# Kernel optimization log

Hardware: AMD Instinct MI355X
Metric: run time of the kernel (lower is better)

The kernel has to match this reference:

```python
import jax, jax.numpy as jnp
import numpy as np

K = 2  # kernel_size == stride (non-overlapping pool)

def setup_inputs() -> dict:
    key = jax.random.key(0)
    x = jax.random.normal(key, (32, 128, 128, 128), dtype=jnp.float32)
    return {"x": x}

def reference(x) -> jnp.ndarray:
    B, C, H, W = x.shape
    h, w = H // K, W // K
    # extract non-overlapping KxK patches: [B,C,h,w,K*K], row-major within window
    p = x.reshape(B, C, h, K, w, K).transpose(0, 1, 2, 4, 3, 5).reshape(B, C, h, w, K * K)
    vals = jnp.max(p, axis=-1)            # pooled values [B,C,h,w]
    idx = jnp.argmax(p, axis=-1)          # in-window flat index (first max, like torch)
    # decode global position of the max element
    row = jnp.arange(h, dtype=jnp.int32)[:, None] * K + (idx // K)  # [B,C,h,w]
    col = jnp.arange(w, dtype=jnp.int32)[None, :] * K + (idx % K)
    pos_h = row.astype(x.dtype) / H
    pos_w = col.astype(x.dtype) / W
    return jnp.concatenate([vals, pos_h, pos_w], axis=1)  # [B, 3C, h, w]
```

## Files before the change

kernel.cpp:

```cpp
#include <hip/hip_runtime.h>


typedef float f32x4 __attribute__((ext_vector_type(4)));
typedef float f32x2 __attribute__((ext_vector_type(2)));

__global__ __launch_bounds__(256) void pap_kernel(const float* __restrict__ x,
                                                  float* __restrict__ out) {
    constexpr int C = 128, H = 128, W = 128;
    constexpr int OH = 64, OW = 64;
    constexpr float inv = 1.0f / 128.0f;
    constexpr int NTILES = 32 * C * (OH / 2);
    constexpr size_t plane = (size_t)C * OH * OW;

    const int lane = threadIdx.x & 63;
    const int wid  = (blockIdx.x * blockDim.x + threadIdx.x) >> 6;
    const int nw   = (gridDim.x * blockDim.x) >> 6;
    const bool hi  = lane >= 32;
    const int j    = lane & 31;

    for (int t = wid; t < NTILES; t += nw) {
        const int oh01 = t & 31;
        const int bc   = t >> 5;

        const size_t base = (size_t)bc * (H * W) + (size_t)oh01 * (4 * W) + lane * 4;
        f32x4 la = __builtin_nontemporal_load(reinterpret_cast<const f32x4*>(x + base));
        f32x4 lb = __builtin_nontemporal_load(reinterpret_cast<const f32x4*>(x + base + 2 * W));

        float top[4], bot[4];
        #pragma unroll
        for (int k = 0; k < 4; ++k) {
            const float sa = __shfl_xor(la[k], 32, 64);
            const float sb = __shfl_xor(lb[k], 32, 64);
            top[k] = hi ? sb : la[k];
            bot[k] = hi ? lb[k] : sa;
        }

        const int oh_out = 2 * oh01 + (hi ? 1 : 0);
        f32x2 vals, ph, pw;
        {
            float v = top[0]; int idx = 0;
            if (top[1] > v) { v = top[1]; idx = 1; }
            if (bot[0] > v) { v = bot[0]; idx = 2; }
            if (bot[1] > v) { v = bot[1]; idx = 3; }
            vals.x = v;
            ph.x = (float)(2 * oh_out + (idx >> 1)) * inv;
            pw.x = (float)(4 * j + (idx & 1)) * inv;
        }
        {
            float v = top[2]; int idx = 0;
            if (top[3] > v) { v = top[3]; idx = 1; }
            if (bot[2] > v) { v = bot[2]; idx = 2; }
            if (bot[3] > v) { v = bot[3]; idx = 3; }
            vals.y = v;
            ph.y = (float)(2 * oh_out + (idx >> 1)) * inv;
            pw.y = (float)(4 * j + 2 + (idx & 1)) * inv;
        }

        const int b_ = bc >> 7, c = bc & (C - 1);
        const size_t orow = ((size_t)(b_ * (3 * C) + c)) * (OH * OW)
                          + (size_t)oh_out * OW + 2 * j;
        __builtin_nontemporal_store(vals, reinterpret_cast<f32x2*>(out + orow));
        __builtin_nontemporal_store(ph,   reinterpret_cast<f32x2*>(out + orow + plane));
        __builtin_nontemporal_store(pw,   reinterpret_cast<f32x2*>(out + orow + 2 * plane));
    }
}

extern "C" void kernel_launch(void* const* d_in, const int* in_sizes, int n_in,
                              void* d_out, int out_size, void* d_ws, size_t ws_size,
                              hipStream_t stream) {
    const float* x = (const float*)d_in[0];
    float* out = (float*)d_out;
    const int blocks = 4096;
    pap_kernel<<<blocks, 256, 0, stream>>>(x, out);
}
```

Baseline: 82.76 us.

## Use fixed per-wave batch stride with hoisted index math and unrolled loads

Result: slower. 87.05 us (+5.2%).

```diff
diff --git a/kernel.cpp b/kernel.cpp
--- a/kernel.cpp
+++ b/kernel.cpp
@@ -9,33 +9,44 @@
     constexpr int C = 128, H = 128, W = 128;
     constexpr int OH = 64, OW = 64;
     constexpr float inv = 1.0f / 128.0f;
-    constexpr int NTILES = 32 * C * (OH / 2);
     constexpr size_t plane = (size_t)C * OH * OW;
+    constexpr int NITER = 16;
+    constexpr size_t IN_STEP  = (size_t)256 * H * W;
+    constexpr size_t OUT_STEP = (size_t)2 * 3 * C * OH * OW;
 
     const int lane = threadIdx.x & 63;
     const int wid  = (blockIdx.x * blockDim.x + threadIdx.x) >> 6;
-    const int nw   = (gridDim.x * blockDim.x) >> 6;
     const bool hi  = lane >= 32;
     const int j    = lane & 31;
 
-    for (int t = wid; t < NTILES; t += nw) {
-        const int oh01 = t & 31;
-        const int bc   = t >> 5;
+    const int oh01 = wid & 31;
+    const int bc0  = wid >> 5;
+    const int b0   = bc0 >> 7, c0 = bc0 & (C - 1);
+    const int oh_out = 2 * oh01 + (hi ? 1 : 0);
 
-        const size_t base = (size_t)bc * (H * W) + (size_t)oh01 * (4 * W) + lane * 4;
+    size_t base = (size_t)bc0 * (H * W) + (size_t)oh01 * (4 * W) + lane * 4;
+    size_t orow = ((size_t)(b0 * (3 * C) + c0)) * (OH * OW)
+                + (size_t)oh_out * OW + 2 * j;
+
+    const float ph_lo = (float)(2 * oh_out) * inv;
+    const float ph_hi = (float)(2 * oh_out + 1) * inv;
+    const float pw0_lo = (float)(4 * j) * inv,     pw0_hi = (float)(4 * j + 1) * inv;
+    const float pw1_lo = (float)(4 * j + 2) * inv, pw1_hi = (float)(4 * j + 3) * inv;
+
+    #pragma unroll 4
+    for (int k = 0; k < NITER; ++k) {
         f32x4 la = __builtin_nontemporal_load(reinterpret_cast<const f32x4*>(x + base));
         f32x4 lb = __builtin_nontemporal_load(reinterpret_cast<const f32x4*>(x + base + 2 * W));
 
         float top[4], bot[4];
         #pragma unroll
-        for (int k = 0; k < 4; ++k) {
-            const float sa = __shfl_xor(la[k], 32, 64);
-            const float sb = __shfl_xor(lb[k], 32, 64);
-            top[k] = hi ? sb : la[k];
-            bot[k] = hi ? lb[k] : sa;
+        for (int e = 0; e < 4; ++e) {
+            const float sa = __shfl_xor(la[e], 32, 64);
+            const float sb = __shfl_xor(lb[e], 32, 64);
+            top[e] = hi ? sb : la[e];
+            bot[e] = hi ? lb[e] : sa;
         }
 
-        const int oh_out = 2 * oh01 + (hi ? 1 : 0);
         f32x2 vals, ph, pw;
         {
             float v = top[0]; int idx = 0;
@@ -43,8 +54,8 @@
             if (bot[0] > v) { v = bot[0]; idx = 2; }
             if (bot[1] > v) { v = bot[1]; idx = 3; }
             vals.x = v;
-            ph.x = (float)(2 * oh_out + (idx >> 1)) * inv;
-            pw.x = (float)(4 * j + (idx & 1)) * inv;
+            ph.x = (idx & 2) ? ph_hi : ph_lo;
+            pw.x = (idx & 1) ? pw0_hi : pw0_lo;
         }
         {
             float v = top[2]; int idx = 0;
@@ -52,16 +63,16 @@
             if (bot[2] > v) { v = bot[2]; idx = 2; }
             if (bot[3] > v) { v = bot[3]; idx = 3; }
             vals.y = v;
-            ph.y = (float)(2 * oh_out + (idx >> 1)) * inv;
-            pw.y = (float)(4 * j + 2 + (idx & 1)) * inv;
+            ph.y = (idx & 2) ? ph_hi : ph_lo;
+            pw.y = (idx & 1) ? pw1_hi : pw1_lo;
         }
 
-        const int b_ = bc >> 7, c = bc & (C - 1);
-        const size_t orow = ((size_t)(b_ * (3 * C) + c)) * (OH * OW)
-                          + (size_t)oh_out * OW + 2 * j;
         __builtin_nontemporal_store(vals, reinterpret_cast<f32x2*>(out + orow));
         __builtin_nontemporal_store(ph,   reinterpret_cast<f32x2*>(out + orow + plane));
         __builtin_nontemporal_store(pw,   reinterpret_cast<f32x2*>(out + orow + 2 * plane));
+
+        base += IN_STEP;
+        orow += OUT_STEP;
     }
 }
 
@@ -70,6 +81,5 @@
                               hipStream_t stream) {
     const float* x = (const float*)d_in[0];
     float* out = (float*)d_out;
-    const int blocks = 4096;
-    pap_kernel<<<blocks, 256, 0, stream>>>(x, out);
+    pap_kernel<<<2048, 256, 0, stream>>>(x, out);
 }
```
